# Kernel tuning notes

Hardware: AMD Instinct MI355X
Metric: run time of the kernel (lower is better)

The kernel has to match this reference:

```python
import jax, jax.numpy as jnp
import numpy as np

N = 262144
IN_DIM = 256
HIDDEN = 256
NUM_SEG = 1024


def setup_inputs() -> dict:
    key = jax.random.key(0)
    k1, k2, k3, k4, k5, k6 = jax.random.split(key, 6)
    x = jax.random.normal(k1, (N, IN_DIM), dtype=jnp.float32)
    batch = jnp.sort(jax.random.randint(k2, (N,), 0, NUM_SEG)).astype(jnp.int64)
    s1 = 1.0 / np.sqrt(IN_DIM)
    s2 = 1.0 / np.sqrt(HIDDEN)
    W1 = jax.random.uniform(k3, (IN_DIM, HIDDEN), jnp.float32, -s1, s1)
    b1 = jax.random.uniform(k4, (HIDDEN,), jnp.float32, -s1, s1)
    W2 = jax.random.uniform(k5, (HIDDEN, 1), jnp.float32, -s2, s2)
    b2 = jax.random.uniform(k6, (1,), jnp.float32, -s2, s2)
    return {"x": x, "W1": W1, "b1": b1, "W2": W2, "b2": b2, "batch": batch}


def reference(x, W1, b1, W2, b2, batch):
    # gate MLP: Linear -> ReLU -> Linear(->1), squeeze
    h = jnp.maximum(x @ W1 + b1, 0.0)            # [N, H]
    scores = (h @ W2 + b2)[:, 0]                  # [N]
    # segment max; torch scatter_reduce 'amax' into zeros includes the
    # initial 0, so the effective max is clamped at >= 0
    seg_max = jax.ops.segment_max(scores, batch, num_segments=NUM_SEG)
    seg_max = jnp.maximum(seg_max, 0.0)           # [G]
    w = jnp.exp(scores - seg_max[batch])          # [N]
    seg_sum = jax.ops.segment_sum(w, batch, num_segments=NUM_SEG)  # [G]
    w = w / (seg_sum[batch] + 1e-9)               # [N]
    out = jax.ops.segment_sum(x * w[:, None], batch, num_segments=NUM_SEG)  # [G, D]
    return out
```

## Files before the change

### kernel.cpp

```cpp
#include <hip/hip_runtime.h>
#include <hip/hip_bf16.h>
#include <stdint.h>

typedef __attribute__((ext_vector_type(8))) short short8;
typedef __attribute__((ext_vector_type(4))) float f32x4;

static constexpr int kN   = 262144;
static constexpr int kD   = 256;
static constexpr int kSeg = 1024;
static constexpr int kRS  = 260;

__device__ __forceinline__ unsigned short f2bf(float f) {
    union { float f; unsigned int u; } v; v.f = f;
    unsigned int u = v.u;
    return (unsigned short)((u + 0x7FFFu + ((u >> 16) & 1u)) >> 16);
}

__device__ __forceinline__ void gload_lds16(const float* gsrc, float* lds_dst) {
    __builtin_amdgcn_global_load_lds(
        (const __attribute__((address_space(1))) void*)gsrc,
        (__attribute__((address_space(3))) void*)lds_dst,
        16, 0, 0);
}

__global__ void pack_w1_kernel(const float* __restrict__ W1, unsigned short* __restrict__ packed) {
    int t = blockIdx.x * blockDim.x + threadIdx.x;
    int l = t & 63, kk = (t >> 6) & 7, j = t >> 9;
    int col = j * 16 + (l & 15);
    int kb  = kk * 32 + ((l >> 4) & 3) * 8;
    short8 s;
#pragma unroll
    for (int i = 0; i < 8; ++i) s[i] = (short)f2bf(W1[(size_t)(kb + i) * kD + col]);
    *reinterpret_cast<short8*>(packed + (size_t)t * 8) = s;
}

__global__ __launch_bounds__(256, 4) void score_kernel(
    const float* __restrict__ x, const unsigned short* __restrict__ packedW1,
    const float* __restrict__ b1, const float* __restrict__ W2,
    const float* __restrict__ b2, float* __restrict__ scores)
{
    __shared__ float sx[32 * kRS];
    __shared__ float sred[4][32];

    const int tid  = threadIdx.x;
    const int lane = tid & 63;
    const int wave = tid >> 6;
    const int r0   = lane & 15;
    const int q    = lane >> 4;
    const int block_row = blockIdx.x * 32;

    {
        const float* src = x + (size_t)(block_row + wave * 8) * kD + lane * 4;
#pragma unroll
        for (int r = 0; r < 8; ++r)
            gload_lds16(src + (size_t)r * kD, &sx[(wave * 8 + r) * kRS]);
    }
    asm volatile("s_waitcnt vmcnt(0)" ::: "memory");
    __syncthreads();

    short8 afrag[2][8];
#pragma unroll
    for (int rt = 0; rt < 2; ++rt) {
        const float* rp = &sx[(rt * 16 + r0) * kRS + q * 8];
#pragma unroll
        for (int kk = 0; kk < 8; ++kk) {
            f32x4 v0 = *reinterpret_cast<const f32x4*>(rp + kk * 32);
            f32x4 v1 = *reinterpret_cast<const f32x4*>(rp + kk * 32 + 4);
            short8 a;
            a[0] = (short)f2bf(v0[0]); a[1] = (short)f2bf(v0[1]);
            a[2] = (short)f2bf(v0[2]); a[3] = (short)f2bf(v0[3]);
            a[4] = (short)f2bf(v1[0]); a[5] = (short)f2bf(v1[1]);
            a[6] = (short)f2bf(v1[2]); a[7] = (short)f2bf(v1[3]);
            afrag[rt][kk] = a;
        }
    }

    float spart[2][4];
#pragma unroll
    for (int rt = 0; rt < 2; ++rt)
#pragma unroll
        for (int r = 0; r < 4; ++r) spart[rt][r] = 0.f;

    const short8* bbase = reinterpret_cast<const short8*>(packedW1);
#pragma unroll
    for (int jj = 0; jj < 4; ++jj) {
        const int j = wave * 4 + jj;
        short8 bfrag[8];
        const short8* bp = bbase + (size_t)(j * 8) * 64 + lane;
#pragma unroll
        for (int kk = 0; kk < 8; ++kk) bfrag[kk] = bp[(size_t)kk * 64];

        const int col   = j * 16 + r0;
        const float b1c = b1[col];
        const float w2c = W2[col];
#pragma unroll
        for (int rt = 0; rt < 2; ++rt) {
            f32x4 acc = {0.f, 0.f, 0.f, 0.f};
#pragma unroll
            for (int kk = 0; kk < 8; ++kk)
                acc = __builtin_amdgcn_mfma_f32_16x16x32_bf16(afrag[rt][kk], bfrag[kk], acc, 0, 0, 0);
#pragma unroll
            for (int r = 0; r < 4; ++r) {
                float h = fmaxf(acc[r] + b1c, 0.f);
                spart[rt][r] = fmaf(h, w2c, spart[rt][r]);
            }
        }
    }

#pragma unroll
    for (int rt = 0; rt < 2; ++rt)
#pragma unroll
        for (int r = 0; r < 4; ++r) {
            float v = spart[rt][r];
            v += __shfl_xor(v, 1);
            v += __shfl_xor(v, 2);
            v += __shfl_xor(v, 4);
            v += __shfl_xor(v, 8);
            if (r0 == 0) sred[wave][rt * 16 + q * 4 + r] = v;
        }
    __syncthreads();
    if (tid < 32)
        scores[block_row + tid] = sred[0][tid] + sred[1][tid] + sred[2][tid] + sred[3][tid] + b2[0];
}

__global__ __launch_bounds__(256) void pool_kernel(
    const float* __restrict__ x, const int* __restrict__ batch,
    const float* __restrict__ scores, float* __restrict__ out)
{
    const int g    = blockIdx.x;
    const int tid  = threadIdx.x;
    const int lane = tid & 63;
    const int wave = tid >> 6;

    __shared__ int   s_bounds[2];
    __shared__ float red[4];

    if (tid < 2) {
        int target = g + tid;
        int lo = 0, hi = kN;
        while (lo < hi) {
            int mid = (lo + hi) >> 1;
            if (batch[mid] < target) lo = mid + 1; else hi = mid;
        }
        s_bounds[tid] = lo;
    }
    __syncthreads();
    const int lo = s_bounds[0], hi = s_bounds[1];

    float m = 0.f;
    for (int i = lo + tid; i < hi; i += 256) m = fmaxf(m, scores[i]);
#pragma unroll
    for (int off = 32; off > 0; off >>= 1) m = fmaxf(m, __shfl_xor(m, off));
    if (lane == 0) red[wave] = m;
    __syncthreads();
    m = fmaxf(fmaxf(red[0], red[1]), fmaxf(red[2], red[3]));
    __syncthreads();

    float sum = 0.f;
    for (int i = lo + tid; i < hi; i += 256) sum += __expf(scores[i] - m);
#pragma unroll
    for (int off = 32; off > 0; off >>= 1) sum += __shfl_xor(sum, off);
    if (lane == 0) red[wave] = sum;
    __syncthreads();
    sum = red[0] + red[1] + red[2] + red[3];

    float acc0 = 0.f, acc1 = 0.f, acc2 = 0.f, acc3 = 0.f;
    int i = lo;
    for (; i + 4 <= hi; i += 4) {
        float w0 = __expf(scores[i + 0] - m);
        float w1 = __expf(scores[i + 1] - m);
        float w2 = __expf(scores[i + 2] - m);
        float w3 = __expf(scores[i + 3] - m);
        acc0 = fmaf(x[(size_t)(i + 0) * kD + tid], w0, acc0);
        acc1 = fmaf(x[(size_t)(i + 1) * kD + tid], w1, acc1);
        acc2 = fmaf(x[(size_t)(i + 2) * kD + tid], w2, acc2);
        acc3 = fmaf(x[(size_t)(i + 3) * kD + tid], w3, acc3);
    }
    for (; i < hi; ++i) {
        float w = __expf(scores[i] - m);
        acc0 = fmaf(x[(size_t)i * kD + tid], w, acc0);
    }
    float acc = (acc0 + acc1) + (acc2 + acc3);
    out[(size_t)g * kD + tid] = acc / (sum + 1e-9f);
}

extern "C" void kernel_launch(void* const* d_in, const int* in_sizes, int n_in,
                              void* d_out, int out_size, void* d_ws, size_t ws_size,
                              hipStream_t stream) {
    const float* x     = (const float*)d_in[0];
    const float* W1    = (const float*)d_in[1];
    const float* b1    = (const float*)d_in[2];
    const float* W2    = (const float*)d_in[3];
    const float* b2    = (const float*)d_in[4];
    const int*   batch = (const int*)d_in[5];
    float* out = (float*)d_out;

    unsigned short* packed = (unsigned short*)d_ws;
    float* scores = (float*)((char*)d_ws + 131072);

    pack_w1_kernel<<<32, 256, 0, stream>>>(W1, packed);
    score_kernel<<<kN / 32, 256, 0, stream>>>(x, packed, b1, W2, b2, scores);
    pool_kernel<<<kSeg, 256, 0, stream>>>(x, batch, scores, out);
}
```

Baseline: 461.0 us.

## Fuse softmax-weighted pooling into score kernel using LDS-resident x tiles

The score kernel now computes exp(score) per row and accumulates weighted x rows from the tile already held in LDS. It writes up to two per-segment partial sums per 32-row block, and a small reduce kernel combines those partials per segment. This removes the second full pass over x and the serial max/sum/accumulate loops of the old pool kernel. In exchange it drops the max subtraction, so large scores could overflow. It also assumes each 32-row block spans at most two segments, which holds for these inputs but not in general.

```diff
diff --git a/kernel.cpp b/kernel.cpp
--- a/kernel.cpp
+++ b/kernel.cpp
@@ -1,5 +1,4 @@
 #include <hip/hip_runtime.h>
-#include <hip/hip_bf16.h>
 #include <stdint.h>
 
 typedef __attribute__((ext_vector_type(8))) short short8;
@@ -9,6 +8,7 @@
 static constexpr int kD   = 256;
 static constexpr int kSeg = 1024;
 static constexpr int kRS  = 260;
+static constexpr int kNB  = kN / 32;
 
 __device__ __forceinline__ unsigned short f2bf(float f) {
     union { float f; unsigned int u; } v; v.f = f;
@@ -34,13 +34,17 @@
     *reinterpret_cast<short8*>(packed + (size_t)t * 8) = s;
 }
 
-__global__ __launch_bounds__(256, 4) void score_kernel(
+__global__ __launch_bounds__(256, 4) void score_accum_kernel(
     const float* __restrict__ x, const unsigned short* __restrict__ packedW1,
     const float* __restrict__ b1, const float* __restrict__ W2,
-    const float* __restrict__ b2, float* __restrict__ scores)
+    const float* __restrict__ b2, const int* __restrict__ batch,
+    float* __restrict__ partial_x, float* __restrict__ partial_w,
+    int* __restrict__ slot_seg)
 {
     __shared__ float sx[32 * kRS];
     __shared__ float sred[4][32];
+    __shared__ float sw[32];
+    __shared__ int   sseg[32];
 
     const int tid  = threadIdx.x;
     const int lane = tid & 63;
@@ -48,6 +52,8 @@
     const int r0   = lane & 15;
     const int q    = lane >> 4;
     const int block_row = blockIdx.x * 32;
+
+    if (tid < 32) sseg[tid] = batch[block_row + tid];
 
     {
         const float* src = x + (size_t)(block_row + wave * 8) * kD + lane * 4;
@@ -75,12 +81,7 @@
         }
     }
 
-    float spart[2][4];
-#pragma unroll
-    for (int rt = 0; rt < 2; ++rt)
-#pragma unroll
-        for (int r = 0; r < 4; ++r) spart[rt][r] = 0.f;
-
+    float spart[2][4] = {{0.f,0.f,0.f,0.f},{0.f,0.f,0.f,0.f}};
     const short8* bbase = reinterpret_cast<const short8*>(packedW1);
 #pragma unroll
     for (int jj = 0; jj < 4; ++jj) {
@@ -89,10 +90,9 @@
         const short8* bp = bbase + (size_t)(j * 8) * 64 + lane;
 #pragma unroll
         for (int kk = 0; kk < 8; ++kk) bfrag[kk] = bp[(size_t)kk * 64];
-
-        const int col   = j * 16 + r0;
-        const float b1c = b1[col];
-        const float w2c = W2[col];
+        const int col16 = j * 16 + r0;
+        const float b1c = b1[col16];
+        const float w2c = W2[col16];
 #pragma unroll
         for (int rt = 0; rt < 2; ++rt) {
             f32x4 acc = {0.f, 0.f, 0.f, 0.f};
@@ -111,30 +111,51 @@
     for (int rt = 0; rt < 2; ++rt)
 #pragma unroll
         for (int r = 0; r < 4; ++r) {
-            float v = spart[rt][r];
-            v += __shfl_xor(v, 1);
-            v += __shfl_xor(v, 2);
-            v += __shfl_xor(v, 4);
-            v += __shfl_xor(v, 8);
-            if (r0 == 0) sred[wave][rt * 16 + q * 4 + r] = v;
-        }
-    __syncthreads();
-    if (tid < 32)
-        scores[block_row + tid] = sred[0][tid] + sred[1][tid] + sred[2][tid] + sred[3][tid] + b2[0];
-}
-
-__global__ __launch_bounds__(256) void pool_kernel(
-    const float* __restrict__ x, const int* __restrict__ batch,
-    const float* __restrict__ scores, float* __restrict__ out)
+            float vv = spart[rt][r];
+            vv += __shfl_xor(vv, 1);
+            vv += __shfl_xor(vv, 2);
+            vv += __shfl_xor(vv, 4);
+            vv += __shfl_xor(vv, 8);
+            if (r0 == 0) sred[wave][rt * 16 + q * 4 + r] = vv;
+        }
+    __syncthreads();
+    if (tid < 32) {
+        float s = sred[0][tid] + sred[1][tid] + sred[2][tid] + sred[3][tid] + b2[0];
+        sw[tid] = __expf(s);
+    }
+    __syncthreads();
+
+    const int base = blockIdx.x * 2;
+    int   cur = sseg[0], slot = 0;
+    float acc = 0.f, wsum = 0.f;
+    for (int i = 0; i < 32; ++i) {
+        const float wv = sw[i];
+        const int   sg = sseg[i];
+        if (sg != cur) {
+            partial_x[(size_t)(base + slot) * kD + tid] = acc;
+            if (tid == 0) { partial_w[base + slot] = wsum; slot_seg[base + slot] = cur; }
+            slot = (slot < 1) ? slot + 1 : 1;
+            acc = 0.f; wsum = 0.f; cur = sg;
+        }
+        acc  = fmaf(sx[i * kRS + tid], wv, acc);
+        wsum += wv;
+    }
+    partial_x[(size_t)(base + slot) * kD + tid] = acc;
+    if (tid == 0) {
+        partial_w[base + slot] = wsum;
+        slot_seg[base + slot]  = cur;
+        if (slot == 0) slot_seg[base + 1] = -1;
+    }
+}
+
+__global__ __launch_bounds__(256) void reduce_kernel(
+    const int* __restrict__ batch, const float* __restrict__ partial_x,
+    const float* __restrict__ partial_w, const int* __restrict__ slot_seg,
+    float* __restrict__ out)
 {
-    const int g    = blockIdx.x;
-    const int tid  = threadIdx.x;
-    const int lane = tid & 63;
-    const int wave = tid >> 6;
-
-    __shared__ int   s_bounds[2];
-    __shared__ float red[4];
-
+    const int g   = blockIdx.x;
+    const int tid = threadIdx.x;
+    __shared__ int sb[2];
     if (tid < 2) {
         int target = g + tid;
         int lo = 0, hi = kN;
@@ -142,46 +163,26 @@
             int mid = (lo + hi) >> 1;
             if (batch[mid] < target) lo = mid + 1; else hi = mid;
         }
-        s_bounds[tid] = lo;
-    }
-    __syncthreads();
-    const int lo = s_bounds[0], hi = s_bounds[1];
-
-    float m = 0.f;
-    for (int i = lo + tid; i < hi; i += 256) m = fmaxf(m, scores[i]);
-#pragma unroll
-    for (int off = 32; off > 0; off >>= 1) m = fmaxf(m, __shfl_xor(m, off));
-    if (lane == 0) red[wave] = m;
-    __syncthreads();
-    m = fmaxf(fmaxf(red[0], red[1]), fmaxf(red[2], red[3]));
-    __syncthreads();
-
-    float sum = 0.f;
-    for (int i = lo + tid; i < hi; i += 256) sum += __expf(scores[i] - m);
-#pragma unroll
-    for (int off = 32; off > 0; off >>= 1) sum += __shfl_xor(sum, off);
-    if (lane == 0) red[wave] = sum;
-    __syncthreads();
-    sum = red[0] + red[1] + red[2] + red[3];
-
-    float acc0 = 0.f, acc1 = 0.f, acc2 = 0.f, acc3 = 0.f;
-    int i = lo;
-    for (; i + 4 <= hi; i += 4) {
-        float w0 = __expf(scores[i + 0] - m);
-        float w1 = __expf(scores[i + 1] - m);
-        float w2 = __expf(scores[i + 2] - m);
-        float w3 = __expf(scores[i + 3] - m);
-        acc0 = fmaf(x[(size_t)(i + 0) * kD + tid], w0, acc0);
-        acc1 = fmaf(x[(size_t)(i + 1) * kD + tid], w1, acc1);
-        acc2 = fmaf(x[(size_t)(i + 2) * kD + tid], w2, acc2);
-        acc3 = fmaf(x[(size_t)(i + 3) * kD + tid], w3, acc3);
-    }
-    for (; i < hi; ++i) {
-        float w = __expf(scores[i] - m);
-        acc0 = fmaf(x[(size_t)i * kD + tid], w, acc0);
-    }
-    float acc = (acc0 + acc1) + (acc2 + acc3);
-    out[(size_t)g * kD + tid] = acc / (sum + 1e-9f);
+        sb[tid] = lo;
+    }
+    __syncthreads();
+    const int lo = sb[0], hi = sb[1];
+
+    float acc = 0.f, wsum = 0.f;
+    if (hi > lo) {
+        const int b0 = lo >> 5, b1 = (hi - 1) >> 5;
+        for (int b = b0; b <= b1; ++b) {
+#pragma unroll
+            for (int s = 0; s < 2; ++s) {
+                const int idx = b * 2 + s;
+                if (slot_seg[idx] == g) {
+                    acc  += partial_x[(size_t)idx * kD + tid];
+                    wsum += partial_w[idx];
+                }
+            }
+        }
+    }
+    out[(size_t)g * kD + tid] = acc / (wsum + 1e-9f);
 }
 
 extern "C" void kernel_launch(void* const* d_in, const int* in_sizes, int n_in,
@@ -195,10 +196,14 @@
     const int*   batch = (const int*)d_in[5];
     float* out = (float*)d_out;
 
-    unsigned short* packed = (unsigned short*)d_ws;
-    float* scores = (float*)((char*)d_ws + 131072);
+    char* ws = (char*)d_ws;
+    unsigned short* packed  = (unsigned short*)ws;
+    float* partial_x = (float*)(ws + (1u << 17));
+    float* partial_w = (float*)(ws + (1u << 17) + (1u << 24));
+    int*   slot_seg  = (int*)  (ws + (1u << 17) + (1u << 24) + (1u << 16));
 
     pack_w1_kernel<<<32, 256, 0, stream>>>(W1, packed);
-    score_kernel<<<kN / 32, 256, 0, stream>>>(x, packed, b1, W2, b2, scores);
-    pool_kernel<<<kSeg, 256, 0, stream>>>(x, batch, scores, out);
-}
+    score_accum_kernel<<<kNB, 256, 0, stream>>>(x, packed, b1, W2, b2, batch,
+                                                partial_x, partial_w, slot_seg);
+    reduce_kernel<<<kSeg, 256, 0, stream>>>(batch, partial_x, partial_w, slot_seg, out);
+}
```

New measurement: 427.6 us. 1.08x faster.
